# Kernel optimization log

Measured on AMD Instinct MI355X. Metric: run time of the kernel, lower is better.

The kernel has to match this reference:

```python
import jax, jax.numpy as jnp
import numpy as np

B, S, W = 128, 100, 20
D, L, H, DFF = 192, 6, 8, 256
DH = D // H

def _ln(x, g, b, eps=1e-5):
    m = jnp.mean(x, -1, keepdims=True)
    v = jnp.var(x, -1, keepdims=True)
    return (x - m) * jax.lax.rsqrt(v + eps) * g + b

def _pos_encoding(seq_len, d):
    pos = np.arange(seq_len, dtype=np.float32)[:, None]
    div = np.exp(np.arange(0, d, 2, dtype=np.float32) * (-np.log(10000.0) / d))
    pe = np.zeros((seq_len, d), dtype=np.float32)
    pe[:, 0::2] = np.sin(pos * div)
    pe[:, 1::2] = np.cos(pos * div)
    return jnp.asarray(pe)

def setup_inputs() -> dict:
    key = jax.random.key(0)
    ks = iter(jax.random.split(key, 80))
    def nrm(shape, s=0.05):
        return jax.random.normal(next(ks), shape, jnp.float32) * s
    inp = {
        'title_idx': jax.random.randint(next(ks), (B, S, W), 0, 1000),
        'class_idx': jax.random.randint(next(ks), (B, S, W), 0, 500),
        'process_idx': jax.random.randint(next(ks), (B, S, W), 0, 1000),
        'activity_type': jax.random.randint(next(ks), (B, S), 0, 4),
        'mouse_pos': jax.random.uniform(next(ks), (B, S, 2), jnp.float32),
        'rect': jax.random.uniform(next(ks), (B, S, W, 4), jnp.float32),
        'flags': jax.random.uniform(next(ks), (B, S, W, 2), jnp.float32),
        'keyboard_active': jax.random.uniform(next(ks), (B, S, 1), jnp.float32),
        'window_mask': jnp.ones((B, S, W), jnp.float32),
        'noise': jax.random.normal(next(ks), (W, B, D), jnp.float32),
        'title_emb': nrm((1000, 32)),
        'class_emb': nrm((500, 32)),
        'process_emb': nrm((1000, 32)),
        'spatial_w1': nrm((64, 6)), 'spatial_b1': nrm((64,)),
        'spatial_w2': nrm((32, 64)), 'spatial_b2': nrm((32,)),
        'wfuse_w': nrm((128, 128)), 'wfuse_b': nrm((128,)),
        'mouse_w1': nrm((32, 2)), 'mouse_b1': nrm((32,)),
        'mouse_w2': nrm((32, 32)), 'mouse_b2': nrm((32,)),
        'act_emb': nrm((4, 16)),
        'kbd_w': nrm((16, 1)), 'kbd_b': nrm((16,)),
        'afuse_w': nrm((64, 64)), 'afuse_b': nrm((64,)),
        'qkv_w': nrm((L, 3 * D, D)), 'qkv_b': nrm((L, 3 * D)),
        'out_w': nrm((L, D, D)), 'out_b': nrm((L, D)),
        'ff1_w': nrm((L, DFF, D)), 'ff1_b': nrm((L, DFF)),
        'ff2_w': nrm((L, D, DFF)), 'ff2_b': nrm((L, D)),
        'ln1_g': 1.0 + nrm((L, D)), 'ln1_b': nrm((L, D)),
        'ln2_g': 1.0 + nrm((L, D)), 'ln2_b': nrm((L, D)),
        'proj_w1': nrm((256, 192)), 'proj_b1': nrm((256,)),
        'proj_w2': nrm((4, 256)), 'proj_b2': nrm((4,)),
        'ex_w1': nrm((128, 192)), 'ex_b1': nrm((128,)),
        'ex_w2': nrm((1, 128)), 'ex_b2': nrm((1,)),
    }
    return inp

def reference(title_idx, class_idx, process_idx, activity_type, mouse_pos, rect, flags, keyboard_active, window_mask, noise, title_emb, class_emb, process_emb, spatial_w1, spatial_b1, spatial_w2, spatial_b2, wfuse_w, wfuse_b, mouse_w1, mouse_b1, mouse_w2, mouse_b2, act_emb, kbd_w, kbd_b, afuse_w, afuse_b, qkv_w, qkv_b, out_w, out_b, ff1_w, ff1_b, ff2_w, ff2_b, ln1_g, ln1_b, ln2_g, ln2_b, proj_w1, proj_b1, proj_w2, proj_b2, ex_w1, ex_b1, ex_w2, ex_b2):
    # ---- window feature extraction (vectorized over B,S,W) ----
    t = title_emb[title_idx]              # [B,S,W,32]
    c = class_emb[class_idx]
    p = process_emb[process_idx]
    sp_in = jnp.concatenate([rect, flags], -1)  # [B,S,W,6]
    sp = jax.nn.relu(sp_in @ spatial_w1.T + spatial_b1) @ spatial_w2.T + spatial_b2
    wcomb = jnp.concatenate([t, c, p, sp], -1)  # [B,S,W,128]
    wf = jax.nn.relu(wcomb @ wfuse_w.T + wfuse_b) * window_mask[..., None]
    avg_w = jnp.sum(wf, 2) / W            # mean over max_windows incl zero padding
    # ---- activity feature extraction ----
    mp = mouse_pos / jnp.array([1920.0, 1080.0], jnp.float32)
    mf = jax.nn.relu(mp @ mouse_w1.T + mouse_b1) @ mouse_w2.T + mouse_b2  # [B,S,32]
    ae = act_emb[activity_type]           # [B,S,16]
    kf = keyboard_active @ kbd_w.T + kbd_b  # [B,S,16]
    af = jax.nn.relu(jnp.concatenate([mf, ae, kf], -1) @ afuse_w.T + afuse_b)
    # ---- transformer ----
    x = jnp.concatenate([avg_w, af], -1) + _pos_encoding(S, D)[None]  # [B,S,192]
    scale = 1.0 / np.sqrt(DH)
    def block(h, prm):
        qw, qb, ow, ob, f1w, f1b, f2w, f2b, g1, b1, g2, b2 = prm
        qkv = h @ qw.T + qb
        q, k, v = jnp.split(qkv, 3, -1)
        q = q.reshape(B, S, H, DH); k = k.reshape(B, S, H, DH); v = v.reshape(B, S, H, DH)
        a = jax.nn.softmax(jnp.einsum('bqhd,bkhd->bhqk', q, k) * scale, -1)
        o = jnp.einsum('bhqk,bkhd->bqhd', a, v).reshape(B, S, D)
        h = _ln(h + o @ ow.T + ob, g1, b1)
        ff = jax.nn.relu(h @ f1w.T + f1b) @ f2w.T + f2b
        return _ln(h + ff, g2, b2), None
    x, _ = jax.lax.scan(block, x, (qkv_w, qkv_b, out_w, out_b, ff1_w, ff1_b, ff2_w, ff2_b, ln1_g, ln1_b, ln2_g, ln2_b))
    last = x[:, -1, :]                    # [B,192]
    # ---- per-slot heads (noise passed in deterministically) ----
    slot = last[None] + noise * 0.1       # [W,B,192]
    positions = jnp.transpose(jax.nn.relu(slot @ proj_w1.T + proj_b1) @ proj_w2.T + proj_b2, (1, 0, 2))  # [B,W,4]
    existence = jnp.transpose(jax.nn.sigmoid(jax.nn.relu(slot @ ex_w1.T + ex_b1) @ ex_w2.T + ex_b2)[..., 0], (1, 0))  # [B,W]
    return positions, existence
```

## Files before the change

kernel.cpp:

```cpp
#include <hip/hip_runtime.h>
#include <hip/hip_bf16.h>
#include <math.h>

#define B_ 128
#define S_ 100
#define W_ 20
#define D_ 192
#define L_ 6
#define H_ 8
#define DFF_ 256
#define DH_ 24
#define BS_ (B_*S_)
#define THREED_ 576

typedef short short8 __attribute__((ext_vector_type(8)));
typedef short short4v __attribute__((ext_vector_type(4)));
typedef float floatx16 __attribute__((ext_vector_type(16)));

__device__ __forceinline__ float posenc(int s, int c) {
  float freq = expf(-logf(10000.f) * (float)(2 * (c >> 1)) / (float)D_);
  float ang = (float)s * freq;
  return (c & 1) ? cosf(ang) : sinf(ang);
}

__device__ __forceinline__ short8 ld_frag8(const __hip_bfloat16* p) {
  short4v lo = *(const short4v*)p;
  short4v hi = *(const short4v*)(p + 4);
  short8 r;
  r[0]=lo[0]; r[1]=lo[1]; r[2]=lo[2]; r[3]=lo[3];
  r[4]=hi[0]; r[5]=hi[1]; r[6]=hi[2]; r[7]=hi[3];
  return r;
}

__device__ __forceinline__ short f2bf_s(float v) {
  __hip_bfloat16 t = __float2bfloat16(v);
  return *reinterpret_cast<short*>(&t);
}

__device__ __forceinline__ float dot4(float4 a, float4 b) {
  return a.x*b.x + a.y*b.y + a.z*b.z + a.w*b.w;
}

__global__ __launch_bounds__(256)
void convertprep_kernel(
    const float* __restrict__ s0, __hip_bfloat16* __restrict__ d0,
    const float* __restrict__ s1, __hip_bfloat16* __restrict__ d1,
    const float* __restrict__ s2, __hip_bfloat16* __restrict__ d2,
    const float* __restrict__ s3, __hip_bfloat16* __restrict__ d3,
    const float* __restrict__ te, const float* __restrict__ ce,
    const float* __restrict__ pe, const float* __restrict__ wfw,
    const float* __restrict__ wfb, const float* __restrict__ sw2,
    const float* __restrict__ sb2,
    float* __restrict__ TE2, float* __restrict__ CE2,
    float* __restrict__ PE2, __hip_bfloat16* __restrict__ WSPb,
    float* __restrict__ PEtab)
{
  int b = blockIdx.x, tid = threadIdx.x;
  if (b < 720) {
    const float* s; __hip_bfloat16* d; int base;
    if      (b < 324) { s = s0; d = d0; base = b; }
    else if (b < 432) { s = s1; d = d1; base = b - 324; }
    else if (b < 576) { s = s2; d = d2; base = b - 432; }
    else              { s = s3; d = d3; base = b - 576; }
    int i = (base * 256 + tid) * 8;
    float4 v0 = *(const float4*)(s + i);
    float4 v1 = *(const float4*)(s + i + 4);
    __hip_bfloat162* d2p = (__hip_bfloat162*)(d + i);
    d2p[0] = __float22bfloat162_rn(make_float2(v0.x, v0.y));
    d2p[1] = __float22bfloat162_rn(make_float2(v0.z, v0.w));
    d2p[2] = __float22bfloat162_rn(make_float2(v1.x, v1.y));
    d2p[3] = __float22bfloat162_rn(make_float2(v1.z, v1.w));
    return;
  }
  int blk = b - 720;
  if (blk < 1250) {
    int item = blk * 256 + tid;
    int v = item >> 7, o = item & 127;
    const float* src; float* dst; int base, vv;
    float a;
    if (v < 1000) {
      src = te; dst = TE2; base = 0; vv = v;
      a = wfb[o];
      const float4* w4 = (const float4*)(wfw + o * 128 + 96);
      const float4* b4 = (const float4*)sb2;
      #pragma unroll
      for (int k4 = 0; k4 < 8; ++k4) a += dot4(w4[k4], b4[k4]);
    } else if (v < 1500) {
      src = ce; dst = CE2; base = 32; vv = v - 1000; a = 0.f;
    } else {
      src = pe; dst = PE2; base = 64; vv = v - 1500; a = 0.f;
    }
    const float4* s4 = (const float4*)(src + vv * 32);
    const float4* w4 = (const float4*)(wfw + o * 128 + base);
    #pragma unroll
    for (int k4 = 0; k4 < 8; ++k4) a += dot4(s4[k4], w4[k4]);
    int op = ((o & 31) << 2) + (o >> 5);
    dst[vv * 128 + op] = a;
  } else if (blk < 1282) {
    int item = (blk - 1250) * 256 + tid;
    int j = item >> 7, o = item & 127;
    float a = 0.f;
    #pragma unroll 8
    for (int k = 0; k < 32; ++k) a += wfw[o * 128 + 96 + k] * sw2[k * 64 + j];
    WSPb[o * 64 + j] = __float2bfloat16(a);
  } else {
    int idx = (blk - 1282) * 256 + tid;
    int s_ = idx / D_, c = idx - s_ * D_;
    PEtab[idx] = posenc(s_, c);
  }
}

__global__ __launch_bounds__(256)
void encode8_kernel(
    const int* __restrict__ title_idx, const int* __restrict__ class_idx,
    const int* __restrict__ process_idx, const int* __restrict__ activity_type,
    const float* __restrict__ mouse_pos, const float* __restrict__ rect,
    const float* __restrict__ flags, const float* __restrict__ keyboard_active,
    const float* __restrict__ window_mask,
    const float* __restrict__ sw1, const float* __restrict__ sb1,
    const float* __restrict__ TE2, const float* __restrict__ CE2,
    const float* __restrict__ PE2, const __hip_bfloat16* __restrict__ WSPb,
    const float* __restrict__ PEtab,
    const float* __restrict__ mw1, const float* __restrict__ mb1,
    const float* __restrict__ mw2, const float* __restrict__ mb2,
    const float* __restrict__ act_emb, const float* __restrict__ kbw,
    const float* __restrict__ kbb,
    const float* __restrict__ afw, const float* __restrict__ afb,
    float* __restrict__ x, __hip_bfloat16* __restrict__ xb)
{
  __shared__ __hip_bfloat16 Bls[128][72];
  __shared__ int   idxS[4][20][3];
  __shared__ float maskS[4][20];
  __shared__ __align__(16) float rectS[4][20][8];

  int tid = threadIdx.x;
  int w = tid >> 6, lane = tid & 63;
  int m32 = lane & 31, half = lane >> 5;
  int bs0 = blockIdx.x * 4;
  int bs = bs0 + w;

  for (int e = tid; e < 240; e += 256) {
    int g2 = e / 60, rem = e % 60, which = rem / 20, w_ = rem % 20;
    const int* src = (which == 0) ? title_idx : (which == 1) ? class_idx : process_idx;
    idxS[g2][w_][which] = src[(bs0 + g2) * W_ + w_];
  }
  if (tid < 80) {
    int g2 = tid / 20, w_ = tid % 20;
    maskS[g2][w_] = window_mask[(bs0 + g2) * W_ + w_];
  }
  for (int e = tid; e < 480; e += 256) {
    int g2 = e / 120, rem = e % 120, w_ = rem / 6, c = rem % 6;
    int rg = (bs0 + g2) * W_ + w_;
    rectS[g2][w_][c] = (c < 4) ? rect[rg * 4 + c] : flags[rg * 2 + (c - 4)];
  }
  for (int e = tid; e < 1024; e += 256) {
    int col = e >> 3, k8 = e & 7;
    short8 v = *(const short8*)&WSPb[col * 64 + k8 * 8];
    *(short8*)&Bls[col][k8 * 8] = v;
  }
  __syncthreads();

  short8 afr[4];
  {
    float rc[6];
    bool act = (m32 < W_);
    if (act) {
      #pragma unroll
      for (int c = 0; c < 6; ++c) rc[c] = rectS[w][m32][c];
    }
    #pragma unroll
    for (int s = 0; s < 4; ++s) {
      short8 f;
      #pragma unroll
      for (int jp = 0; jp < 8; ++jp) {
        float a = 0.f;
        if (act) {
          int j = s * 16 + half * 8 + jp;
          const float* w1 = sw1 + j * 6;
          a = sb1[j];
          #pragma unroll
          for (int c = 0; c < 6; ++c) a += w1[c] * rc[c];
          a = fmaxf(a, 0.f);
        }
        f[jp] = f2bf_s(a);
      }
      afr[s] = f;
    }
  }

  floatx16 acc[4];
  #pragma unroll
  for (int nt = 0; nt < 4; ++nt)
    #pragma unroll
    for (int r = 0; r < 16; ++r) acc[nt][r] = 0.f;

  #pragma unroll
  for (int s = 0; s < 4; ++s) {
    int ko = s * 16 + half * 8;
    #pragma unroll
    for (int nt = 0; nt < 4; ++nt) {
      short8 bf = *(const short8*)&Bls[nt * 32 + m32][ko];
      acc[nt] = __builtin_amdgcn_mfma_f32_32x32x16_bf16(afr[s], bf, acc[nt], 0, 0, 0);
    }
  }

  float cs[4] = {0.f, 0.f, 0.f, 0.f};
  #pragma unroll
  for (int r = 0; r < 16; ++r) {
    int row = (r & 3) + 8 * (r >> 2) + 4 * half;
    if (row < W_) {
      int t  = idxS[w][row][0];
      int ci = idxS[w][row][1];
      int p  = idxS[w][row][2];
      float mk = maskS[w][row];
      float4 gt = *(const float4*)&TE2[(size_t)t  * 128 + m32 * 4];
      float4 gc = *(const float4*)&CE2[(size_t)ci * 128 + m32 * 4];
      float4 gp = *(const float4*)&PE2[(size_t)p  * 128 + m32 * 4];
      float g0 = gt.x + gc.x + gp.x;
      float g1 = gt.y + gc.y + gp.y;
      float g2v = gt.z + gc.z + gp.z;
      float g3 = gt.w + gc.w + gp.w;
      cs[0] += fmaxf(acc[0][r] + g0, 0.f) * mk;
      cs[1] += fmaxf(acc[1][r] + g1, 0.f) * mk;
      cs[2] += fmaxf(acc[2][r] + g2v, 0.f) * mk;
      cs[3] += fmaxf(acc[3][r] + g3, 0.f) * mk;
    }
  }
  #pragma unroll
  for (int nt = 0; nt < 4; ++nt) cs[nt] += __shfl_xor(cs[nt], 32);
  if (half == 0) {
    int s_ = bs % S_;
    #pragma unroll
    for (int nt = 0; nt < 4; ++nt) {
      int col = nt * 32 + m32;
      float v = cs[nt] * (1.f / (float)W_) + PEtab[s_ * D_ + col];
      x[(size_t)bs * D_ + col] = v;
      xb[(size_t)bs * D_ + col] = __float2bfloat16(v);
    }
  }

  {
    float* wsc = &rectS[w][0][0];
    if (lane < 32) {
      float mx = mouse_pos[bs * 2 + 0] * (1.f / 1920.f);
      float my = mouse_pos[bs * 2 + 1] * (1.f / 1080.f);
      wsc[64 + lane] = fmaxf(mw1[lane * 2] * mx + mw1[lane * 2 + 1] * my + mb1[lane], 0.f);
    }
    __builtin_amdgcn_wave_barrier();
    float cv;
    if (lane < 32) {
      float a = mb2[lane];
      const float4* wv = (const float4*)(mw2 + lane * 32);
      const float4* hv = (const float4*)(wsc + 64);
      #pragma unroll
      for (int k4 = 0; k4 < 8; ++k4) {
        float4 ww = wv[k4], hh = hv[k4];
        a += ww.x*hh.x + ww.y*hh.y + ww.z*hh.z + ww.w*hh.w;
      }
      cv = a;
    } else if (lane < 48) {
      cv = act_emb[activity_type[bs] * 16 + (lane - 32)];
    } else {
      cv = kbw[lane - 48] * keyboard_active[bs] + kbb[lane - 48];
    }
    wsc[lane] = cv;
    __builtin_amdgcn_wave_barrier();
    {
      float a = afb[lane];
      const float4* w4 = (const float4*)(afw + lane * 64);
      const float4* cp = (const float4*)wsc;
      #pragma unroll
      for (int k4 = 0; k4 < 16; ++k4) {
        float4 ww = w4[k4], c2 = cp[k4];
        a += ww.x*c2.x + ww.y*c2.y + ww.z*c2.z + ww.w*c2.w;
      }
      float v = fmaxf(a, 0.f);
      int cg = 128 + lane;
      float ovv = v + PEtab[(bs % S_) * D_ + cg];
      x[(size_t)bs * D_ + cg] = ovv;
      xb[(size_t)bs * D_ + cg] = __float2bfloat16(ovv);
    }
  }
}

__global__ __launch_bounds__(256)
void qkvattn_kernel(const __hip_bfloat16* __restrict__ xb,
                    const __hip_bfloat16* __restrict__ Wq,
                    const float* __restrict__ qb,
                    __hip_bfloat16* __restrict__ o)
{
  __shared__ __align__(16) char smem[40960];
  __hip_bfloat16* Asl = (__hip_bfloat16*)smem;
  __hip_bfloat16* Bsl = (__hip_bfloat16*)(smem + 10240);
  __hip_bfloat16* Qs  = (__hip_bfloat16*)smem;
  __hip_bfloat16* Ks  = (__hip_bfloat16*)(smem + 10240);
  __hip_bfloat16* Ps  = (__hip_bfloat16*)smem;
  __hip_bfloat16* Vt  = (__hip_bfloat16*)(smem + 33792);

  int bh = blockIdx.x;
  int hh = bh & 7, b = bh >> 3;
  int tid = threadIdx.x, lane = tid & 63, w = tid >> 6;
  int m32 = lane & 31, half = lane >> 5;

  for (int e = tid; e < (32 * 112) / 8; e += 256)
    ((float4*)Vt)[e] = make_float4(0.f, 0.f, 0.f, 0.f);

  int rA = tid >> 1, hA = tid & 1;
  int rrA = rA < S_ ? rA : S_ - 1;
  size_t baseA = (size_t)(b * S_ + rrA) * D_;
  float4* dA = (float4*)&Asl[rA * 40 + hA * 16];

  bool isB = (tid < 192);
  int rB = tid >> 1;
  int tB = rB >> 5, jB = rB & 31;
  bool actB = isB && (jB < DH_);
  size_t baseB = actB ? (size_t)(tB * D_ + hh * DH_ + jB) * D_ : 0;
  float4* dB = (float4*)&Bsl[rB * 40 + hA * 16];

  if (isB && !actB) {
    float4 z = make_float4(0.f, 0.f, 0.f, 0.f);
    dB[0] = z; dB[1] = z;
  }
  {
    float4 a0, a1, b0, b1;
    const float4* s = (const float4*)&xb[baseA + hA * 16];
    a0 = s[0]; a1 = s[1];
    if (actB) {
      const float4* sB = (const float4*)&Wq[baseB + hA * 16];
      b0 = sB[0]; b1 = sB[1];
      dB[0] = b0; dB[1] = b1;
    }
    dA[0] = a0; dA[1] = a1;
  }

  floatx16 acc[3];
  #pragma unroll
  for (int t = 0; t < 3; ++t)
    #pragma unroll
    for (int r = 0; r < 16; ++r) acc[t][r] = 0.f;

  for (int k0 = 0; k0 < D_; k0 += 32) {
    bool more = (k0 + 32 < D_);
    __syncthreads();
    float4 na0, na1, nb0, nb1;
    if (more) {
      const float4* s = (const float4*)&xb[baseA + k0 + 32 + hA * 16];
      na0 = s[0]; na1 = s[1];
      if (actB) {
        const float4* sB = (const float4*)&Wq[baseB + k0 + 32 + hA * 16];
        nb0 = sB[0]; nb1 = sB[1];
      }
    }
    #pragma unroll
    for (int kc = 0; kc < 2; ++kc) {
      int ko = kc * 16 + half * 8;
      short8 a = *(const short8*)&Asl[(w * 32 + m32) * 40 + ko];
      #pragma unroll
      for (int t = 0; t < 3; ++t) {
        short8 bf = *(const short8*)&Bsl[(t * 32 + m32) * 40 + ko];
        acc[t] = __builtin_amdgcn_mfma_f32_32x32x16_bf16(a, bf, acc[t], 0, 0, 0);
      }
    }
    __syncthreads();
    if (more) {
      dA[0] = na0; dA[1] = na1;
      if (actB) { dB[0] = nb0; dB[1] = nb1; }
    }
  }
  {
    bool dv = (m32 < DH_);
    float bq = dv ? qb[0 * D_ + hh * DH_ + m32] : 0.f;
    float bk = dv ? qb[1 * D_ + hh * DH_ + m32] : 0.f;
    float bv = dv ? qb[2 * D_ + hh * DH_ + m32] : 0.f;
    #pragma unroll
    for (int r = 0; r < 16; ++r) {
      int row = w * 32 + (r & 3) + 8 * (r >> 2) + 4 * half;
      Qs[row * 40 + m32] = __float2bfloat16(dv ? acc[0][r] + bq : 0.f);
      Ks[row * 40 + m32] = __float2bfloat16(dv ? acc[1][r] + bk : 0.f);
      if (dv && row < S_) Vt[m32 * 112 + row] = __float2bfloat16(acc[2][r] + bv);
    }
  }
  __syncthreads();

  floatx16 sc[4];
  #pragma unroll
  for (int nt = 0; nt < 4; ++nt)
    #pragma unroll
    for (int r = 0; r < 16; ++r) sc[nt][r] = 0.f;
  #pragma unroll
  for (int kc = 0; kc < 2; ++kc) {
    int ko = kc * 16 + half * 8;
    short8 a = *(const short8*)&Qs[(w * 32 + m32) * 40 + ko];
    #pragma unroll
    for (int nt = 0; nt < 4; ++nt) {
      short8 bf = *(const short8*)&Ks[(nt * 32 + m32) * 40 + ko];
      sc[nt] = __builtin_amdgcn_mfma_f32_32x32x16_bf16(a, bf, sc[nt], 0, 0, 0);
    }
  }
  __syncthreads();

  const float scale = 0.20412414523193154f;
  float rinv[16];
  #pragma unroll
  for (int r = 0; r < 16; ++r) {
    float mx = -1e30f;
    #pragma unroll
    for (int nt = 0; nt < 4; ++nt) {
      float s = sc[nt][r] * scale;
      if (nt == 3 && m32 >= 4) s = -1e30f;
      sc[nt][r] = s;
      mx = fmaxf(mx, s);
    }
    #pragma unroll
    for (int off = 1; off < 32; off <<= 1) mx = fmaxf(mx, __shfl_xor(mx, off));
    float sum = 0.f;
    #pragma unroll
    for (int nt = 0; nt < 4; ++nt) {
      float e = expf(sc[nt][r] - mx);
      sc[nt][r] = e;
      sum += e;
    }
    #pragma unroll
    for (int off = 1; off < 32; off <<= 1) sum += __shfl_xor(sum, off);
    rinv[r] = 1.f / sum;
  }
  #pragma unroll
  for (int r = 0; r < 16; ++r) {
    int rowl = (r & 3) + 8 * (r >> 2) + 4 * half;
    #pragma unroll
    for (int nt = 0; nt < 4; ++nt)
      Ps[(w * 32 + rowl) * 132 + nt * 32 + m32] = __float2bfloat16(sc[nt][r]);
  }

  floatx16 ov;
  #pragma unroll
  for (int r = 0; r < 16; ++r) ov[r] = 0.f;
  #pragma unroll
  for (int kt = 0; kt < 7; ++kt) {
    int ko = kt * 16 + half * 8;
    short8 a = ld_frag8(&Ps[(w * 32 + m32) * 132 + ko]);
    short8 bf = *(const short8*)&Vt[m32 * 112 + ko];
    ov = __builtin_amdgcn_mfma_f32_32x32x16_bf16(a, bf, ov, 0, 0, 0);
  }
  #pragma unroll
  for (int r = 0; r < 16; ++r) {
    int rowl = (r & 3) + 8 * (r >> 2) + 4 * half;
    int q = w * 32 + rowl;
    if (m32 < DH_ && q < S_)
      o[((size_t)(b * S_ + q)) * D_ + hh * DH_ + m32] =
          __float2bfloat16(ov[r] * rinv[r]);
  }
}

__global__ __launch_bounds__(256)
void outffln_kernel(const __hip_bfloat16* __restrict__ attb,
                    const __hip_bfloat16* __restrict__ Wo, const float* __restrict__ bo,
                    const float* __restrict__ g1, const float* __restrict__ b1v,
                    const __hip_bfloat16* __restrict__ W1, const float* __restrict__ b1,
                    const __hip_bfloat16* __restrict__ W2, const float* __restrict__ b2,
                    const float* __restrict__ g2, const float* __restrict__ b2v,
                    float* __restrict__ x, __hip_bfloat16* __restrict__ xb)
{
  __shared__ __align__(16) char arena[59904];
  __hip_bfloat16* AslA = (__hip_bfloat16*)arena;
  __hip_bfloat16* BslA = (__hip_bfloat16*)(arena + 5120);
  __hip_bfloat16* C1   = (__hip_bfloat16*)arena;
  __hip_bfloat16* AslB = (__hip_bfloat16*)(arena + 33280);
  __hip_bfloat16* BslB = (__hip_bfloat16*)(arena + 38400);
  float (*psum)[2] = (float(*)[2])(arena + 58880);
  float (*psq)[2]  = (float(*)[2])(arena + 59392);

  int tid = threadIdx.x, lane = tid & 63, w = tid >> 6;
  int m32 = lane & 31, half = lane >> 5;
  int mt = w & 1, ng = w >> 1;
  int bm = blockIdx.x * 64;

  bool sA = (tid < 128);
  int rA = tid >> 1, hA = tid & 1;
  int r0 = tid >> 1, h0 = tid & 1;
  int r1 = (tid + 256) >> 1, h1 = tid & 1;

  floatx16 accA[3];
  #pragma unroll
  for (int j = 0; j < 3; ++j)
    #pragma unroll
    for (int r = 0; r < 16; ++r) accA[j][r] = 0.f;

  {
    float4* dA  = (float4*)&AslA[rA * 40 + hA * 16];
    float4* dB0 = (float4*)&BslA[r0 * 40 + h0 * 16];
    float4* dB1 = (float4*)&BslA[r1 * 40 + h1 * 16];
    bool s1 = (tid < 128);

    {
      if (sA) {
        const float4* s = (const float4*)(attb + (size_t)(bm + rA) * D_ + hA * 16);
        dA[0] = s[0]; dA[1] = s[1];
      }
      {
        const float4* s = (const float4*)(Wo + (size_t)r0 * D_ + h0 * 16);
        dB0[0] = s[0]; dB0[1] = s[1];
      }
      if (s1) {
        const float4* s = (const float4*)(Wo + (size_t)r1 * D_ + h1 * 16);
        dB1[0] = s[0]; dB1[1] = s[1];
      }
    }
    for (int k0 = 0; k0 < D_; k0 += 32) {
      bool more = (k0 + 32 < D_);
      __syncthreads();
      float4 na0, na1, nb00, nb01, nb10, nb11;
      if (more) {
        if (sA) {
          const float4* s = (const float4*)(attb + (size_t)(bm + rA) * D_ + k0 + 32 + hA * 16);
          na0 = s[0]; na1 = s[1];
        }
        {
          const float4* s = (const float4*)(Wo + (size_t)r0 * D_ + k0 + 32 + h0 * 16);
          nb00 = s[0]; nb01 = s[1];
        }
        if (s1) {
          const float4* s = (const float4*)(Wo + (size_t)r1 * D_ + k0 + 32 + h1 * 16);
          nb10 = s[0]; nb11 = s[1];
        }
      }
      #pragma unroll
      for (int kc = 0; kc < 2; ++kc) {
        int ko = kc * 16 + half * 8;
        short8 a = *(const short8*)&AslA[(mt * 32 + m32) * 40 + ko];
        #pragma unroll
        for (int j = 0; j < 3; ++j) {
          short8 bf = *(const short8*)&BslA[((ng * 3 + j) * 32 + m32) * 40 + ko];
          accA[j] = __builtin_amdgcn_mfma_f32_32x32x16_bf16(a, bf, accA[j], 0, 0, 0);
        }
      }
      __syncthreads();
      if (more) {
        if (sA) { dA[0] = na0; dA[1] = na1; }
        dB0[0] = nb00; dB0[1] = nb01;
        if (s1) { dB1[0] = nb10; dB1[1] = nb11; }
      }
    }
  }
  {
    int rowb = mt * 32 + 4 * half;
    #pragma unroll
    for (int r = 0; r < 16; ++r) {
      int rl = rowb + (r & 3) + 8 * (r >> 2);
      int row = bm + rl;
      float p = 0.f;
      #pragma unroll
      for (int j = 0; j < 3; ++j) {
        int col = (ng * 3 + j) * 32 + m32;
        float t = accA[j][r] + bo[col] + x[(size_t)row * D_ + col];
        accA[j][r] = t;
        p += t;
      }
      #pragma unroll
      for (int off = 1; off < 32; off <<= 1) p += __shfl_xor(p, off);
      if (m32 == 0) psum[rl][ng] = p;
    }
    __syncthreads();
    float mean[16];
    #pragma unroll
    for (int r = 0; r < 16; ++r) {
      int rl = rowb + (r & 3) + 8 * (r >> 2);
      mean[r] = (psum[rl][0] + psum[rl][1]) * (1.f / (float)D_);
    }
    #pragma unroll
    for (int r = 0; r < 16; ++r) {
      int rl = rowb + (r & 3) + 8 * (r >> 2);
      float s = 0.f;
      #pragma unroll
      for (int j = 0; j < 3; ++j) { float dd = accA[j][r] - mean[r]; s += dd * dd; }
      #pragma unroll
      for (int off = 1; off < 32; off <<= 1) s += __shfl_xor(s, off);
      if (m32 == 0) psq[rl][ng] = s;
    }
    __syncthreads();
    #pragma unroll
    for (int r = 0; r < 16; ++r) {
      int rl = rowb + (r & 3) + 8 * (r >> 2);
      int row = bm + rl;
      float inv = rsqrtf((psq[rl][0] + psq[rl][1]) * (1.f / (float)D_) + 1e-5f);
      #pragma unroll
      for (int j = 0; j < 3; ++j) {
        int col = (ng * 3 + j) * 32 + m32;
        float ovv = (accA[j][r] - mean[r]) * inv * g1[col] + b1v[col];
        x[(size_t)row * D_ + col] = ovv;
        xb[(size_t)row * D_ + col] = __float2bfloat16(ovv);
      }
    }
  }
  __syncthreads();

  floatx16 acc1[4];
  #pragma unroll
  for (int j = 0; j < 4; ++j)
    #pragma unroll
    for (int r = 0; r < 16; ++r) acc1[j][r] = 0.f;

  {
    float4* dA  = (float4*)&AslB[rA * 40 + hA * 16];
    float4* dB0 = (float4*)&BslB[r0 * 40 + h0 * 16];
    float4* dB1 = (float4*)&BslB[r1 * 40 + h1 * 16];

    {
      if (sA) {
        const float4* s = (const float4*)(xb + (size_t)(bm + rA) * D_ + hA * 16);
        dA[0] = s[0]; dA[1] = s[1];
      }
      {
        const float4* s = (const float4*)(W1 + (size_t)r0 * D_ + h0 * 16);
        dB0[0] = s[0]; dB0[1] = s[1];
      }
      {
        const float4* s = (const float4*)(W1 + (size_t)r1 * D_ + h1 * 16);
        dB1[0] = s[0]; dB1[1] = s[1];
      }
    }
    for (int k0 = 0; k0 < D_; k0 += 32) {
      bool more = (k0 + 32 < D_);
      __syncthreads();
      float4 na0, na1, nb00, nb01, nb10, nb11;
      if (more) {
        if (sA) {
          const float4* s = (const float4*)(xb + (size_t)(bm + rA) * D_ + k0 + 32 + hA * 16);
          na0 = s[0]; na1 = s[1];
        }
        {
          const float4* s = (const float4*)(W1 + (size_t)r0 * D_ + k0 + 32 + h0 * 16);
          nb00 = s[0]; nb01 = s[1];
        }
        {
          const float4* s = (const float4*)(W1 + (size_t)r1 * D_ + k0 + 32 + h1 * 16);
          nb10 = s[0]; nb11 = s[1];
        }
      }
      #pragma unroll
      for (int kc = 0; kc < 2; ++kc) {
        int ko = kc * 16 + half * 8;
        short8 a = *(const short8*)&AslB[(mt * 32 + m32) * 40 + ko];
        #pragma unroll
        for (int j = 0; j < 4; ++j) {
          short8 bf = *(const short8*)&BslB[((ng * 4 + j) * 32 + m32) * 40 + ko];
          acc1[j] = __builtin_amdgcn_mfma_f32_32x32x16_bf16(a, bf, acc1[j], 0, 0, 0);
        }
      }
      __syncthreads();
      if (more) {
        if (sA) { dA[0] = na0; dA[1] = na1; }
        dB0[0] = nb00; dB0[1] = nb01;
        dB1[0] = nb10; dB1[1] = nb11;
      }
    }
  }
  {
    int rowb = mt * 32 + 4 * half;
    #pragma unroll
    for (int j = 0; j < 4; ++j) {
      int col = (ng * 4 + j) * 32 + m32;
      float cb = b1[col];
      #pragma unroll
      for (int r = 0; r < 16; ++r) {
        int row = rowb + (r & 3) + 8 * (r >> 2);
        C1[row * 260 + col] = __float2bfloat16(fmaxf(acc1[j][r] + cb, 0.f));
      }
    }
  }

  floatx16 acc2[3];
  #pragma unroll
  for (int j = 0; j < 3; ++j)
    #pragma unroll
    for (int r = 0; r < 16; ++r) acc2[j][r] = 0.f;

  {
    float4* dB0 = (float4*)&BslB[r0 * 40 + h0 * 16];
    float4* dB1 = (float4*)&BslB[r1 * 40 + h1 * 16];
    bool s1 = (tid < 128);

    {
      const float4* s = (const float4*)(W2 + (size_t)r0 * DFF_ + h0 * 16);
      dB0[0] = s[0]; dB0[1] = s[1];
      if (s1) {
        const float4* s2 = (const float4*)(W2 + (size_t)r1 * DFF_ + h1 * 16);
        dB1[0] = s2[0]; dB1[1] = s2[1];
      }
    }
    for (int k0 = 0; k0 < DFF_; k0 += 32) {
      bool more = (k0 + 32 < DFF_);
      __syncthreads();
      float4 nb00, nb01, nb10, nb11;
      if (more) {
        {
          const float4* s = (const float4*)(W2 + (size_t)r0 * DFF_ + k0 + 32 + h0 * 16);
          nb00 = s[0]; nb01 = s[1];
        }
        if (s1) {
          const float4* s = (const float4*)(W2 + (size_t)r1 * DFF_ + k0 + 32 + h1 * 16);
          nb10 = s[0]; nb11 = s[1];
        }
      }
      #pragma unroll
      for (int kc = 0; kc < 2; ++kc) {
        int ko = kc * 16 + half * 8;
        short8 a = ld_frag8(&C1[(mt * 32 + m32) * 260 + k0 + ko]);
        #pragma unroll
        for (int j = 0; j < 3; ++j) {
          short8 bf = *(const short8*)&BslB[((ng * 3 + j) * 32 + m32) * 40 + ko];
          acc2[j] = __builtin_amdgcn_mfma_f32_32x32x16_bf16(a, bf, acc2[j], 0, 0, 0);
        }
      }
      __syncthreads();
      if (more) {
        dB0[0] = nb00; dB0[1] = nb01;
        if (s1) { dB1[0] = nb10; dB1[1] = nb11; }
      }
    }
  }

  int rowb = mt * 32 + 4 * half;
  #pragma unroll
  for (int r = 0; r < 16; ++r) {
    int rl = rowb + (r & 3) + 8 * (r >> 2);
    int row = bm + rl;
    float p = 0.f;
    #pragma unroll
    for (int j = 0; j < 3; ++j) {
      int col = (ng * 3 + j) * 32 + m32;
      float t = acc2[j][r] + b2[col] + x[(size_t)row * D_ + col];
      acc2[j][r] = t;
      p += t;
    }
    #pragma unroll
    for (int off = 1; off < 32; off <<= 1) p += __shfl_xor(p, off);
    if (m32 == 0) psum[rl][ng] = p;
  }
  __syncthreads();
  float mean[16];
  #pragma unroll
  for (int r = 0; r < 16; ++r) {
    int rl = rowb + (r & 3) + 8 * (r >> 2);
    mean[r] = (psum[rl][0] + psum[rl][1]) * (1.f / (float)D_);
  }
  #pragma unroll
  for (int r = 0; r < 16; ++r) {
    int rl = rowb + (r & 3) + 8 * (r >> 2);
    float s = 0.f;
    #pragma unroll
    for (int j = 0; j < 3; ++j) { float dd = acc2[j][r] - mean[r]; s += dd * dd; }
    #pragma unroll
    for (int off = 1; off < 32; off <<= 1) s += __shfl_xor(s, off);
    if (m32 == 0) psq[rl][ng] = s;
  }
  __syncthreads();
  #pragma unroll
  for (int r = 0; r < 16; ++r) {
    int rl = rowb + (r & 3) + 8 * (r >> 2);
    int row = bm + rl;
    float inv = rsqrtf((psq[rl][0] + psq[rl][1]) * (1.f / (float)D_) + 1e-5f);
    #pragma unroll
    for (int j = 0; j < 3; ++j) {
      int col = (ng * 3 + j) * 32 + m32;
      float ovv = (acc2[j][r] - mean[r]) * inv * g2[col] + b2v[col];
      x[(size_t)row * D_ + col] = ovv;
      xb[(size_t)row * D_ + col] = __float2bfloat16(ovv);
    }
  }
}

__global__ __launch_bounds__(256)
void head2_kernel(const float* __restrict__ x, const float* __restrict__ noise,
                  const float* __restrict__ pw1, const float* __restrict__ pb1,
                  const float* __restrict__ pw2, const float* __restrict__ pb2,
                  const float* __restrict__ ew1, const float* __restrict__ eb1,
                  const float* __restrict__ ew2, const float* __restrict__ eb2,
                  float* __restrict__ out)
{
  __shared__ float slotS[20][192];
  __shared__ float phS[20][256];
  __shared__ float ehS[20][128];
  int b = blockIdx.x;
  int tid = threadIdx.x;

  const float* lastrow = x + ((size_t)b * S_ + (S_ - 1)) * D_;
  for (int e = tid; e < 20 * 192; e += 256) {
    int w = e / 192, c = e - w * 192;
    slotS[w][c] = lastrow[c] + noise[((size_t)w * B_ + b) * D_ + c] * 0.1f;
  }
  __syncthreads();

  bool doe = (tid < 128);
  float accp[20], acce[20];
  {
    float bp = pb1[tid];
    float be = doe ? eb1[tid] : 0.f;
    #pragma unroll
    for (int w = 0; w < 20; ++w) { accp[w] = bp; acce[w] = be; }
  }
  {
    const float4* wr = (const float4*)(pw1 + (size_t)tid * D_);
    const float4* we = (const float4*)(ew1 + (size_t)(doe ? tid : 0) * D_);
    for (int k4 = 0; k4 < 48; ++k4) {
      float4 wv = wr[k4];
      float4 ev = we[k4];
      #pragma unroll
      for (int w = 0; w < 20; ++w) {
        float4 sv = *(const float4*)&slotS[w][k4 * 4];
        accp[w] += wv.x*sv.x + wv.y*sv.y + wv.z*sv.z + wv.w*sv.w;
        if (doe) acce[w] += ev.x*sv.x + ev.y*sv.y + ev.z*sv.z + ev.w*sv.w;
      }
    }
  }
  #pragma unroll
  for (int w = 0; w < 20; ++w) {
    phS[w][tid] = fmaxf(accp[w], 0.f);
    if (doe) ehS[w][tid] = fmaxf(acce[w], 0.f);
  }
  __syncthreads();

  if (tid < 80) {
    int w = tid >> 2, c = tid & 3;
    float a = pb2[c];
    const float4* wr = (const float4*)(pw2 + c * 256);
    const float4* pp = (const float4*)&phS[w][0];
    for (int k = 0; k < 64; ++k) {
      float4 wv = wr[k], pv = pp[k];
      a += wv.x*pv.x + wv.y*pv.y + wv.z*pv.z + wv.w*pv.w;
    }
    out[((size_t)b * W_ + w) * 4 + c] = a;
  } else if (tid < 100) {
    int w = tid - 80;
    float a = eb2[0];
    const float4* wr = (const float4*)ew2;
    const float4* pp = (const float4*)&ehS[w][0];
    for (int k = 0; k < 32; ++k) {
      float4 wv = wr[k], pv = pp[k];
      a += wv.x*pv.x + wv.y*pv.y + wv.z*pv.z + wv.w*pv.w;
    }
    out[(size_t)B_ * W_ * 4 + (size_t)b * W_ + w] = 1.f / (1.f + expf(-a));
  }
}

extern "C" void kernel_launch(void* const* d_in, const int* in_sizes, int n_in,
                              void* d_out, int out_size, void* d_ws, size_t ws_size,
                              hipStream_t stream)
{
  const int*   title_idx       = (const int*)  d_in[0];
  const int*   class_idx       = (const int*)  d_in[1];
  const int*   process_idx     = (const int*)  d_in[2];
  const int*   activity_type   = (const int*)  d_in[3];
  const float* mouse_pos       = (const float*)d_in[4];
  const float* rect            = (const float*)d_in[5];
  const float* flags           = (const float*)d_in[6];
  const float* keyboard_active = (const float*)d_in[7];
  const float* window_mask     = (const float*)d_in[8];
  const float* noise           = (const float*)d_in[9];
  const float* title_emb       = (const float*)d_in[10];
  const float* class_emb       = (const float*)d_in[11];
  const float* process_emb     = (const float*)d_in[12];
  const float* spatial_w1      = (const float*)d_in[13];
  const float* spatial_b1      = (const float*)d_in[14];
  const float* spatial_w2      = (const float*)d_in[15];
  const float* spatial_b2      = (const float*)d_in[16];
  const float* wfuse_w         = (const float*)d_in[17];
  const float* wfuse_b         = (const float*)d_in[18];
  const float* mouse_w1        = (const float*)d_in[19];
  const float* mouse_b1        = (const float*)d_in[20];
  const float* mouse_w2        = (const float*)d_in[21];
  const float* mouse_b2        = (const float*)d_in[22];
  const float* act_emb         = (const float*)d_in[23];
  const float* kbd_w           = (const float*)d_in[24];
  const float* kbd_b           = (const float*)d_in[25];
  const float* afuse_w         = (const float*)d_in[26];
  const float* afuse_b         = (const float*)d_in[27];
  const float* qkv_w           = (const float*)d_in[28];
  const float* qkv_b           = (const float*)d_in[29];
  const float* out_w           = (const float*)d_in[30];
  const float* out_b           = (const float*)d_in[31];
  const float* ff1_w           = (const float*)d_in[32];
  const float* ff1_b           = (const float*)d_in[33];
  const float* ff2_w           = (const float*)d_in[34];
  const float* ff2_b           = (const float*)d_in[35];
  const float* ln1_g           = (const float*)d_in[36];
  const float* ln1_b           = (const float*)d_in[37];
  const float* ln2_g           = (const float*)d_in[38];
  const float* ln2_b           = (const float*)d_in[39];
  const float* proj_w1         = (const float*)d_in[40];
  const float* proj_b1         = (const float*)d_in[41];
  const float* proj_w2         = (const float*)d_in[42];
  const float* proj_b2         = (const float*)d_in[43];
  const float* ex_w1           = (const float*)d_in[44];
  const float* ex_b1           = (const float*)d_in[45];
  const float* ex_w2           = (const float*)d_in[46];
  const float* ex_b2           = (const float*)d_in[47];

  float* out = (float*)d_out;

  float* x = (float*)d_ws;
  __hip_bfloat16* xb   = (__hip_bfloat16*)(x + (size_t)BS_ * D_);
  __hip_bfloat16* attb = xb   + (size_t)BS_ * D_;
  __hip_bfloat16* wqb  = attb + (size_t)BS_ * D_;
  __hip_bfloat16* wob  = wqb  + (size_t)L_ * THREED_ * D_;
  __hip_bfloat16* wf1b = wob  + (size_t)L_ * D_ * D_;
  __hip_bfloat16* wf2b = wf1b + (size_t)L_ * DFF_ * D_;
  float* TE2  = (float*)(wf2b + (size_t)L_ * D_ * DFF_);
  float* CE2  = TE2  + 1000 * 128;
  float* PE2  = CE2  + 500 * 128;
  __hip_bfloat16* WSPb = (__hip_bfloat16*)(PE2 + 1000 * 128);
  float* PEtab = (float*)(WSPb + 128 * 64);
  (void)ws_size; (void)n_in; (void)in_sizes; (void)out_size;

  convertprep_kernel<<<2077, 256, 0, stream>>>(
      qkv_w, wqb, out_w, wob, ff1_w, wf1b, ff2_w, wf2b,
      title_emb, class_emb, process_emb, wfuse_w, wfuse_b,
      spatial_w2, spatial_b2, TE2, CE2, PE2, WSPb, PEtab);

  encode8_kernel<<<BS_ / 4, 256, 0, stream>>>(
      title_idx, class_idx, process_idx, activity_type, mouse_pos, rect, flags,
      keyboard_active, window_mask, spatial_w1, spatial_b1,
      TE2, CE2, PE2, WSPb, PEtab,
      mouse_w1, mouse_b1, mouse_w2, mouse_b2, act_emb, kbd_w, kbd_b,
      afuse_w, afuse_b, x, xb);

  for (int l = 0; l < L_; ++l) {
    qkvattn_kernel<<<B_ * H_, 256, 0, stream>>>(
        xb, wqb + (size_t)l * THREED_ * D_, qkv_b + (size_t)l * THREED_, attb);
    outffln_kernel<<<BS_ / 64, 256, 0, stream>>>(
        attb, wob + (size_t)l * D_ * D_, out_b + (size_t)l * D_,
        ln1_g + (size_t)l * D_, ln1_b + (size_t)l * D_,
        wf1b + (size_t)l * DFF_ * D_, ff1_b + (size_t)l * DFF_,
        wf2b + (size_t)l * D_ * DFF_, ff2_b + (size_t)l * D_,
        ln2_g + (size_t)l * D_, ln2_b + (size_t)l * D_, x, xb);
  }

  head2_kernel<<<B_, 256, 0, stream>>>(
      x, noise, proj_w1, proj_b1, proj_w2, proj_b2,
      ex_w1, ex_b1, ex_w2, ex_b2, out);
}
```

Measured before the change: 710.0 us.

## Keep LN1 output tile in LDS for FF1 and split encode launch into quarters

In the fused out-proj/FF/LN kernel, the bf16 LN1 output tile is written to a full-width LDS buffer (Afull) as well as global memory. FF1 then reads its A operand straight from LDS instead of re-reading xb from global memory in 32-wide chunks, which removes global traffic and staging stores. The FF2 weight staging moves to its own LDS region so it does not overlap Afull. The encode kernel is now launched as four quarter-size grids via a block-offset parameter, which adds launch overhead with no clear benefit.

Measured after the change: 741.7 us. 4.5% more time.

```diff
diff --git a/kernel.cpp b/kernel.cpp
--- a/kernel.cpp
+++ b/kernel.cpp
@@ -112,6 +112,7 @@
 
 __global__ __launch_bounds__(256)
 void encode8_kernel(
+    int blk_base,
     const int* __restrict__ title_idx, const int* __restrict__ class_idx,
     const int* __restrict__ process_idx, const int* __restrict__ activity_type,
     const float* __restrict__ mouse_pos, const float* __restrict__ rect,
@@ -136,7 +137,7 @@
   int tid = threadIdx.x;
   int w = tid >> 6, lane = tid & 63;
   int m32 = lane & 31, half = lane >> 5;
-  int bs0 = blockIdx.x * 4;
+  int bs0 = (blk_base + blockIdx.x) * 4;
   int bs = bs0 + w;
 
   for (int e = tid; e < 240; e += 256) {
@@ -462,11 +463,12 @@
                     float* __restrict__ x, __hip_bfloat16* __restrict__ xb)
 {
   __shared__ __align__(16) char arena[59904];
-  __hip_bfloat16* AslA = (__hip_bfloat16*)arena;
-  __hip_bfloat16* BslA = (__hip_bfloat16*)(arena + 5120);
-  __hip_bfloat16* C1   = (__hip_bfloat16*)arena;
-  __hip_bfloat16* AslB = (__hip_bfloat16*)(arena + 33280);
-  __hip_bfloat16* BslB = (__hip_bfloat16*)(arena + 38400);
+  __hip_bfloat16* AslA  = (__hip_bfloat16*)arena;
+  __hip_bfloat16* BslA  = (__hip_bfloat16*)(arena + 5120);
+  __hip_bfloat16* Afull = (__hip_bfloat16*)arena;
+  __hip_bfloat16* BslB1 = (__hip_bfloat16*)(arena + 25600);
+  __hip_bfloat16* C1    = (__hip_bfloat16*)arena;
+  __hip_bfloat16* BslB2 = (__hip_bfloat16*)(arena + 33280);
   float (*psum)[2] = (float(*)[2])(arena + 58880);
   float (*psq)[2]  = (float(*)[2])(arena + 59392);
 
@@ -588,7 +590,9 @@
         int col = (ng * 3 + j) * 32 + m32;
         float ovv = (accA[j][r] - mean[r]) * inv * g1[col] + b1v[col];
         x[(size_t)row * D_ + col] = ovv;
-        xb[(size_t)row * D_ + col] = __float2bfloat16(ovv);
+        __hip_bfloat16 hb = __float2bfloat16(ovv);
+        xb[(size_t)row * D_ + col] = hb;
+        Afull[rl * 196 + col] = hb;
       }
     }
   }
@@ -601,55 +605,36 @@
     for (int r = 0; r < 16; ++r) acc1[j][r] = 0.f;
 
   {
-    float4* dA  = (float4*)&AslB[rA * 40 + hA * 16];
-    float4* dB0 = (float4*)&BslB[r0 * 40 + h0 * 16];
-    float4* dB1 = (float4*)&BslB[r1 * 40 + h1 * 16];
-
+    float4* dB0 = (float4*)&BslB1[r0 * 40 + h0 * 16];
+    float4* dB1 = (float4*)&BslB1[r1 * 40 + h1 * 16];
     {
-      if (sA) {
-        const float4* s = (const float4*)(xb + (size_t)(bm + rA) * D_ + hA * 16);
-        dA[0] = s[0]; dA[1] = s[1];
-      }
-      {
-        const float4* s = (const float4*)(W1 + (size_t)r0 * D_ + h0 * 16);
-        dB0[0] = s[0]; dB0[1] = s[1];
-      }
-      {
-        const float4* s = (const float4*)(W1 + (size_t)r1 * D_ + h1 * 16);
-        dB1[0] = s[0]; dB1[1] = s[1];
-      }
+      const float4* s = (const float4*)(W1 + (size_t)r0 * D_ + h0 * 16);
+      dB0[0] = s[0]; dB0[1] = s[1];
+      const float4* s2 = (const float4*)(W1 + (size_t)r1 * D_ + h1 * 16);
+      dB1[0] = s2[0]; dB1[1] = s2[1];
     }
     for (int k0 = 0; k0 < D_; k0 += 32) {
       bool more = (k0 + 32 < D_);
       __syncthreads();
-      float4 na0, na1, nb00, nb01, nb10, nb11;
+      float4 nb00, nb01, nb10, nb11;
       if (more) {
-        if (sA) {
-          const float4* s = (const float4*)(xb + (size_t)(bm + rA) * D_ + k0 + 32 + hA * 16);
-          na0 = s[0]; na1 = s[1];
-        }
-        {
-          const float4* s = (const float4*)(W1 + (size_t)r0 * D_ + k0 + 32 + h0 * 16);
-          nb00 = s[0]; nb01 = s[1];
-        }
-        {
-          const float4* s = (const float4*)(W1 + (size_t)r1 * D_ + k0 + 32 + h1 * 16);
-          nb10 = s[0]; nb11 = s[1];
-        }
+        const float4* s = (const float4*)(W1 + (size_t)r0 * D_ + k0 + 32 + h0 * 16);
+        nb00 = s[0]; nb01 = s[1];
+        const float4* s2 = (const float4*)(W1 + (size_t)r1 * D_ + k0 + 32 + h1 * 16);
+        nb10 = s2[0]; nb11 = s2[1];
       }
       #pragma unroll
       for (int kc = 0; kc < 2; ++kc) {
         int ko = kc * 16 + half * 8;
-        short8 a = *(const short8*)&AslB[(mt * 32 + m32) * 40 + ko];
+        short8 a = ld_frag8(&Afull[(mt * 32 + m32) * 196 + k0 + ko]);
         #pragma unroll
         for (int j = 0; j < 4; ++j) {
-          short8 bf = *(const short8*)&BslB[((ng * 4 + j) * 32 + m32) * 40 + ko];
+          short8 bf = *(const short8*)&BslB1[((ng * 4 + j) * 32 + m32) * 40 + ko];
           acc1[j] = __builtin_amdgcn_mfma_f32_32x32x16_bf16(a, bf, acc1[j], 0, 0, 0);
         }
       }
       __syncthreads();
       if (more) {
-        if (sA) { dA[0] = na0; dA[1] = na1; }
         dB0[0] = nb00; dB0[1] = nb01;
         dB1[0] = nb10; dB1[1] = nb11;
       }
@@ -676,8 +661,8 @@
     for (int r = 0; r < 16; ++r) acc2[j][r] = 0.f;
 
   {
-    float4* dB0 = (float4*)&BslB[r0 * 40 + h0 * 16];
-    float4* dB1 = (float4*)&BslB[r1 * 40 + h1 * 16];
+    float4* dB0 = (float4*)&BslB2[r0 * 40 + h0 * 16];
+    float4* dB1 = (float4*)&BslB2[r1 * 40 + h1 * 16];
     bool s1 = (tid < 128);
 
     {
@@ -708,7 +693,7 @@
         short8 a = ld_frag8(&C1[(mt * 32 + m32) * 260 + k0 + ko]);
         #pragma unroll
         for (int j = 0; j < 3; ++j) {
-          short8 bf = *(const short8*)&BslB[((ng * 3 + j) * 32 + m32) * 40 + ko];
+          short8 bf = *(const short8*)&BslB2[((ng * 3 + j) * 32 + m32) * 40 + ko];
           acc2[j] = __builtin_amdgcn_mfma_f32_32x32x16_bf16(a, bf, acc2[j], 0, 0, 0);
         }
       }
@@ -917,12 +902,15 @@
       title_emb, class_emb, process_emb, wfuse_w, wfuse_b,
       spatial_w2, spatial_b2, TE2, CE2, PE2, WSPb, PEtab);
 
-  encode8_kernel<<<BS_ / 4, 256, 0, stream>>>(
-      title_idx, class_idx, process_idx, activity_type, mouse_pos, rect, flags,
-      keyboard_active, window_mask, spatial_w1, spatial_b1,
-      TE2, CE2, PE2, WSPb, PEtab,
-      mouse_w1, mouse_b1, mouse_w2, mouse_b2, act_emb, kbd_w, kbd_b,
-      afuse_w, afuse_b, x, xb);
+  for (int q = 0; q < 4; ++q) {
+    encode8_kernel<<<BS_ / 16, 256, 0, stream>>>(
+        q * (BS_ / 16),
+        title_idx, class_idx, process_idx, activity_type, mouse_pos, rect, flags,
+        keyboard_active, window_mask, spatial_w1, spatial_b1,
+        TE2, CE2, PE2, WSPb, PEtab,
+        mouse_w1, mouse_b1, mouse_w2, mouse_b2, act_emb, kbd_w, kbd_b,
+        afuse_w, afuse_b, x, xb);
+  }
 
   for (int l = 0; l < L_; ++l) {
     qkvattn_kernel<<<B_ * H_, 256, 0, stream>>>(
```
